# Optimization experiments

Measured on AMD Instinct MI355X. Metric: run time of the kernel, lower is better.

The kernel has to match this reference:

```python
import jax, jax.numpy as jnp
import numpy as np

IN_FEATURES = 1024
OUT_FEATURES = 1024
GRID_SIZE = 5
SPLINE_ORDER = 3
GRID_RANGE = (-1.0, 1.0)


def make_grid():
    h = (GRID_RANGE[1] - GRID_RANGE[0]) / GRID_SIZE
    knots = jnp.arange(-SPLINE_ORDER, GRID_SIZE + SPLINE_ORDER + 1, dtype=jnp.float32) * h + GRID_RANGE[0]
    return jnp.broadcast_to(knots, (IN_FEATURES, knots.shape[0]))  # (in, 12)


def b_splines(x, knots, p):
    # x: (B, in); knots: (in, nk). Cox-de Boor recursion, degree p.
    xs = x[:, :, None]                                   # (B, in, 1)
    bases = ((xs >= knots[None, :, :-1]) & (xs < knots[None, :, 1:])).astype(x.dtype)
    for k in range(1, p + 1):
        den1 = knots[:, k:-1] - knots[:, :-(k + 1)]
        den1 = jnp.where(den1 == 0, jnp.float32(1e-8), den1)
        den2 = knots[:, k + 1:] - knots[:, 1:-k]
        den2 = jnp.where(den2 == 0, jnp.float32(1e-8), den2)
        term1 = (xs - knots[None, :, :-(k + 1)]) / den1[None] * bases[:, :, :-1]
        term2 = (knots[None, :, k + 1:] - xs) / den2[None] * bases[:, :, 1:]
        bases = term1 + term2
    return bases  # (B, in, grid_size + p)


def setup_inputs() -> dict:
    key = jax.random.key(0)
    k1, k2, k3, k4 = jax.random.split(key, 4)
    K = GRID_SIZE + SPLINE_ORDER
    x = jax.random.normal(k1, (4096, IN_FEATURES), dtype=jnp.float32)
    base_weight = jax.random.normal(k2, (OUT_FEATURES, IN_FEATURES), dtype=jnp.float32) * (1.0 / np.sqrt(IN_FEATURES))
    spline_weight = jax.random.normal(k3, (OUT_FEATURES, IN_FEATURES, K), dtype=jnp.float32) * 0.02
    spline_scaler = jax.random.normal(k4, (OUT_FEATURES, IN_FEATURES), dtype=jnp.float32) * (1.0 / np.sqrt(IN_FEATURES))
    grid = make_grid()
    return {"x": x, "base_weight": base_weight, "spline_weight": spline_weight,
            "spline_scaler": spline_scaler, "grid": grid}


def reference(x, base_weight, spline_weight, spline_scaler, grid):
    base_out = jax.nn.silu(x) @ base_weight.T                      # (B, out)
    bases = b_splines(x, grid, SPLINE_ORDER)                       # (B, in, K)
    scaled_sw = spline_weight * spline_scaler[:, :, None]          # (out, in, K)
    spline_out = jnp.einsum('bik,oik->bo', bases, scaled_sw)       # (B, out)
    return base_out + spline_out
```

## Files before the change

### kernel.cpp

```cpp
#include <hip/hip_runtime.h>
#include <hip/hip_bf16.h>
#include <cstdint>
#include <cstddef>

#define AS1 __attribute__((address_space(1)))
#define AS3 __attribute__((address_space(3)))

typedef __bf16 bf16;
typedef __bf16 bf16x4 __attribute__((ext_vector_type(4)));
typedef __bf16 bf16x8 __attribute__((ext_vector_type(8)));
typedef float f32x4 __attribute__((ext_vector_type(4)));

static constexpr int M_ROWS = 4096;
static constexpr int N_COLS = 1024;
static constexpr int IN_F   = 1024;
static constexpr int K2     = IN_F * 9;
static constexpr int BK     = 32;
static constexpr int KT_CNT = K2 / BK;

static constexpr int GBK = 64;
static constexpr int GKT = K2 / GBK;


__device__ __forceinline__ void bases8(float x, float w8[8]) {
  float mf = x * 2.5f + 5.5f;
  int   m  = (int)floorf(mf);
  float u  = mf - (float)m;
  float u2 = u * u, u3 = u2 * u;
  float omu = 1.0f - u;
  const float s = 1.0f / 6.0f;
  float p0 = u3 * s;
  float p1 = (-3.f*u3 + 3.f*u2 + 3.f*u + 1.f) * s;
  float p2 = (3.f*u3 - 6.f*u2 + 4.f) * s;
  float p3 = omu * omu * omu * s;
  bool in = (m >= 0) && (m < 11);
#pragma unroll
  for (int j = 0; j < 8; ++j) {
    float v = 0.0f;
    v = (j == m)     ? p0 : v;
    v = (j == m - 1) ? p1 : v;
    v = (j == m - 2) ? p2 : v;
    v = (j == m - 3) ? p3 : v;
    w8[j] = in ? v : 0.0f;
  }
}

__global__ __launch_bounds__(256) void prep4(
    const float* __restrict__ x, const float* __restrict__ bw,
    const float* __restrict__ sw, const float* __restrict__ sc,
    bf16* __restrict__ A, bf16* __restrict__ BT) {
  const int bid = blockIdx.x;
  if (bid < (M_ROWS * IN_F) / (4 * 256)) {
    const int t  = bid * 256 + threadIdx.x;
    const int b  = t >> 8;
    const int i0 = (t & 255) * 4;
    const float4 xv4 = *(const float4*)(x + (size_t)b * IN_F + i0);
    const float xs[4] = {xv4.x, xv4.y, xv4.z, xv4.w};

    bf16x4 sil;
    bf16* arow = A + (size_t)b * K2;
#pragma unroll
    for (int j = 0; j < 4; ++j) {
      float xv = xs[j];
      sil[j] = (bf16)(xv / (1.0f + __expf(-xv)));
      float w8[8];
      bases8(xv, w8);
      bf16x8 outv;
#pragma unroll
      for (int k = 0; k < 8; ++k) outv[k] = (bf16)w8[k];
      *(bf16x8*)(arow + IN_F + (size_t)(i0 + j) * 8) = outv;
    }
    *(bf16x4*)(arow + i0) = sil;
  } else {
    const int t  = (bid - (M_ROWS * IN_F) / (4 * 256)) * 256 + threadIdx.x;
    const int o  = t >> 8;
    const int i0 = (t & 255) * 4;
    const float4 bv4 = *(const float4*)(bw + (size_t)o * IN_F + i0);
    const float4 sc4 = *(const float4*)(sc + (size_t)o * IN_F + i0);
    const float bs[4] = {bv4.x, bv4.y, bv4.z, bv4.w};
    const float ss[4] = {sc4.x, sc4.y, sc4.z, sc4.w};

    bf16x4 base;
    bf16* brow = BT + (size_t)o * K2;
#pragma unroll
    for (int j = 0; j < 4; ++j) {
      base[j] = (bf16)bs[j];
      const float4* swp = (const float4*)(sw + ((size_t)o * IN_F + i0 + j) * 8);
      float4 a = swp[0], c = swp[1];
      float wv[8] = {a.x, a.y, a.z, a.w, c.x, c.y, c.z, c.w};
      bf16x8 r;
#pragma unroll
      for (int k = 0; k < 8; ++k) r[k] = (bf16)(wv[k] * ss[j]);
      *(bf16x8*)(brow + IN_F + (size_t)(i0 + j) * 8) = r;
    }
    *(bf16x4*)(brow + i0) = base;
  }
}

__device__ __forceinline__ void expand_body(const float* __restrict__ x,
                                            bf16* __restrict__ A, int gid, int r0) {
  int b = gid >> 10;
  int i = gid & 1023;
  float xv = x[(size_t)r0 * IN_F + (size_t)gid];
  A[(size_t)b * K2 + i] = (bf16)(xv / (1.0f + __expf(-xv)));
  float w8[8];
  bases8(xv, w8);
  bf16x8 outv;
#pragma unroll
  for (int j = 0; j < 8; ++j) outv[j] = (bf16)w8[j];
  *(bf16x8*)(A + (size_t)b * K2 + IN_F + (size_t)i * 8) = outv;
}

__device__ __forceinline__ void makebt_body(const float* __restrict__ bw,
                                            const float* __restrict__ sw,
                                            const float* __restrict__ sc,
                                            bf16* __restrict__ BT, int gid) {
  int o = gid >> 10;
  int i = gid & 1023;
  BT[(size_t)o * K2 + i] = (bf16)bw[gid];
  float scale = sc[gid];
  const float4* swp = (const float4*)(sw + (size_t)gid * 8);
  float4 a = swp[0], b4 = swp[1];
  float wv[8] = {a.x, a.y, a.z, a.w, b4.x, b4.y, b4.z, b4.w};
  bf16x8 r;
#pragma unroll
  for (int j = 0; j < 8; ++j) r[j] = (bf16)(wv[j] * scale);
  *(bf16x8*)(BT + (size_t)o * K2 + IN_F + (size_t)i * 8) = r;
}

__global__ void expand_a(const float* __restrict__ x, bf16* __restrict__ A, int r0) {
  expand_body(x, A, blockIdx.x * blockDim.x + threadIdx.x, r0);
}
__global__ void make_bt(const float* __restrict__ bw, const float* __restrict__ sw,
                        const float* __restrict__ sc, bf16* __restrict__ BT) {
  makebt_body(bw, sw, sc, BT, blockIdx.x * blockDim.x + threadIdx.x);
}

__global__ __launch_bounds__(512, 2) void gemm256_8p(
    const bf16* __restrict__ A, const bf16* __restrict__ BT,
    float* __restrict__ P, int kt_seg) {
  __shared__ bf16 As[2][256 * GBK];
  __shared__ bf16 Bs[2][256 * GBK];

  const int tid  = threadIdx.x;
  const int lane = tid & 63;
  const int w    = tid >> 6;

  const int b     = blockIdx.x;
  const int mtile = b & 15;
  const int np    = (b >> 4) & 3;
  const int seg   = b >> 6;
  const int row0  = mtile * 256;
  const int col0  = np * 256;
  const int kt0   = seg * kt_seg;
  float* __restrict__ dst = P + (size_t)seg * M_ROWS * N_COLS;

  const int srow = lane >> 3;
  const int sch  = ((lane & 7) ^ srow) * 8;

  const int r  = lane & 15;
  const int q  = lane >> 4;
  const int wm = (w >> 2) * 128;
  const int wn = (w & 3) * 64;
  const int kc0 = ((0 + q) ^ (r & 7)) * 8;
  const int kc1 = ((4 + q) ^ (r & 7)) * 8;

  const bf16* aB = A  + (size_t)row0 * K2;
  const bf16* bB = BT + (size_t)col0 * K2;

  f32x4 acc[8][4];
#pragma unroll
  for (int mt = 0; mt < 8; ++mt)
#pragma unroll
    for (int nt = 0; nt < 4; ++nt)
      acc[mt][nt] = f32x4{0.f, 0.f, 0.f, 0.f};

  auto stageA = [&](int sbuf, int h, int kt) {
#pragma unroll
    for (int t8 = 0; t8 < 2; ++t8) {
      const int rg = h * 128 + w * 16 + t8 * 8;
      const bf16* ga = aB + (size_t)(rg + srow) * K2 + kt * GBK + sch;
      __builtin_amdgcn_global_load_lds((const AS1 void*)ga,
                                       (AS3 void*)&As[sbuf][rg * GBK], 16, 0, 0);
    }
  };
  auto stageB = [&](int sbuf, int h, int kt) {
#pragma unroll
    for (int t8 = 0; t8 < 2; ++t8) {
      const int rg = h * 128 + w * 16 + t8 * 8;
      const bf16* gb = bB + (size_t)(rg + srow) * K2 + kt * GBK + sch;
      __builtin_amdgcn_global_load_lds((const AS1 void*)gb,
                                       (AS3 void*)&Bs[sbuf][rg * GBK], 16, 0, 0);
    }
  };

  stageA(0, 0, kt0); stageA(0, 1, kt0);
  stageB(0, 0, kt0); stageB(0, 1, kt0);
  if (kt_seg > 1) stageA(1, 0, kt0 + 1);
  if (kt_seg > 1) asm volatile("s_waitcnt vmcnt(2)" ::: "memory");
  else            asm volatile("s_waitcnt vmcnt(0)" ::: "memory");
  __builtin_amdgcn_s_barrier();

  bf16x8 af[4][2], bfr[4][2];

  for (int t = 0; t < kt_seg; ++t) {
    const int buf = t & 1, nbuf = buf ^ 1;
    const bf16* as = As[buf];
    const bf16* bs = Bs[buf];
    const bool sN = (t + 1 < kt_seg);

#pragma unroll
    for (int j = 0; j < 4; ++j) {
      const bf16* ar = &as[(wm + j * 16 + r) * GBK];
      af[j][0] = *(const bf16x8*)&ar[kc0];
      af[j][1] = *(const bf16x8*)&ar[kc1];
    }
#pragma unroll
    for (int j = 0; j < 2; ++j) {
      const bf16* br = &bs[(wn + j * 16 + r) * GBK];
      bfr[j][0] = *(const bf16x8*)&br[kc0];
      bfr[j][1] = *(const bf16x8*)&br[kc1];
    }
    if (sN) stageA(nbuf, 1, kt0 + t + 1);
    asm volatile("s_waitcnt lgkmcnt(8)" ::: "memory");
    __builtin_amdgcn_s_barrier();
    asm volatile("s_waitcnt lgkmcnt(0)" ::: "memory");
    __builtin_amdgcn_sched_barrier(0);
    __builtin_amdgcn_s_setprio(1);
#pragma unroll
    for (int j = 0; j < 4; ++j)
#pragma unroll
      for (int n = 0; n < 2; ++n) {
        acc[j][n] = __builtin_amdgcn_mfma_f32_16x16x32_bf16(af[j][0], bfr[n][0], acc[j][n], 0, 0, 0);
        acc[j][n] = __builtin_amdgcn_mfma_f32_16x16x32_bf16(af[j][1], bfr[n][1], acc[j][n], 0, 0, 0);
      }
    __builtin_amdgcn_s_setprio(0);
    __builtin_amdgcn_s_barrier();

#pragma unroll
    for (int j = 0; j < 2; ++j) {
      const bf16* br = &bs[(wn + (2 + j) * 16 + r) * GBK];
      bfr[2 + j][0] = *(const bf16x8*)&br[kc0];
      bfr[2 + j][1] = *(const bf16x8*)&br[kc1];
    }
    if (sN) stageB(nbuf, 0, kt0 + t + 1);
    __builtin_amdgcn_s_barrier();
    asm volatile("s_waitcnt lgkmcnt(0)" ::: "memory");
    __builtin_amdgcn_sched_barrier(0);
    __builtin_amdgcn_s_setprio(1);
#pragma unroll
    for (int j = 0; j < 4; ++j)
#pragma unroll
      for (int n = 0; n < 2; ++n) {
        acc[j][2 + n] = __builtin_amdgcn_mfma_f32_16x16x32_bf16(af[j][0], bfr[2 + n][0], acc[j][2 + n], 0, 0, 0);
        acc[j][2 + n] = __builtin_amdgcn_mfma_f32_16x16x32_bf16(af[j][1], bfr[2 + n][1], acc[j][2 + n], 0, 0, 0);
      }
    __builtin_amdgcn_s_setprio(0);
    __builtin_amdgcn_s_barrier();

#pragma unroll
    for (int j = 0; j < 4; ++j) {
      const bf16* ar = &as[(wm + (4 + j) * 16 + r) * GBK];
      af[j][0] = *(const bf16x8*)&ar[kc0];
      af[j][1] = *(const bf16x8*)&ar[kc1];
    }
    if (sN) stageB(nbuf, 1, kt0 + t + 1);
    __builtin_amdgcn_s_barrier();
    asm volatile("s_waitcnt lgkmcnt(0)" ::: "memory");
    __builtin_amdgcn_sched_barrier(0);
    __builtin_amdgcn_s_setprio(1);
#pragma unroll
    for (int j = 0; j < 4; ++j)
#pragma unroll
      for (int n = 0; n < 2; ++n) {
        acc[4 + j][n] = __builtin_amdgcn_mfma_f32_16x16x32_bf16(af[j][0], bfr[n][0], acc[4 + j][n], 0, 0, 0);
        acc[4 + j][n] = __builtin_amdgcn_mfma_f32_16x16x32_bf16(af[j][1], bfr[n][1], acc[4 + j][n], 0, 0, 0);
      }
    __builtin_amdgcn_s_setprio(0);
    __builtin_amdgcn_s_barrier();

    if (t + 2 < kt_seg) stageA(buf, 0, kt0 + t + 2);
    if (sN) {
      if (t + 2 < kt_seg) asm volatile("s_waitcnt vmcnt(2)" ::: "memory");
      else                asm volatile("s_waitcnt vmcnt(0)" ::: "memory");
    }
    __builtin_amdgcn_s_barrier();
    __builtin_amdgcn_s_setprio(1);
#pragma unroll
    for (int j = 0; j < 4; ++j)
#pragma unroll
      for (int n = 0; n < 2; ++n) {
        acc[4 + j][2 + n] = __builtin_amdgcn_mfma_f32_16x16x32_bf16(af[j][0], bfr[2 + n][0], acc[4 + j][2 + n], 0, 0, 0);
        acc[4 + j][2 + n] = __builtin_amdgcn_mfma_f32_16x16x32_bf16(af[j][1], bfr[2 + n][1], acc[4 + j][2 + n], 0, 0, 0);
      }
    __builtin_amdgcn_s_setprio(0);
    __builtin_amdgcn_s_barrier();
  }

#pragma unroll
  for (int mt = 0; mt < 8; ++mt)
#pragma unroll
    for (int nt = 0; nt < 4; ++nt)
#pragma unroll
      for (int k = 0; k < 4; ++k) {
        int row = row0 + wm + mt * 16 + q * 4 + k;
        int col = col0 + wn + nt * 16 + r;
        dst[(size_t)row * N_COLS + col] = acc[mt][nt][k];
      }
}

__global__ __launch_bounds__(256, 2) void gemm_fused(
    const bf16* __restrict__ A, const bf16* __restrict__ BT,
    float* __restrict__ d0, float* __restrict__ d1,
    int r0, int mt_cnt, int kt_seg) {
  __shared__ bf16 As[2][128 * GBK];
  __shared__ bf16 Bs[2][128 * GBK];

  const int tid  = threadIdx.x;
  const int lane = tid & 63;
  const int w    = tid >> 6;

  const int bps = mt_cnt * 8;
  int b   = blockIdx.x;
  const int seg = b / bps;
  b -= seg * bps;
  const int row0 = (b % mt_cnt) * 128;
  const int col0 = (b / mt_cnt) * 128;
  float* __restrict__ dst = seg ? d1 : d0;
  const int kt0 = seg * kt_seg;

  const int srow = lane >> 3;
  const int sch  = ((lane & 7) ^ srow) * 8;
  const int r  = lane & 15;
  const int q  = lane >> 4;
  const int wm = (w >> 1) * 64;
  const int wn = (w & 1) * 64;
  const int kc0 = ((0 + q) ^ (r & 7)) * 8;
  const int kc1 = ((4 + q) ^ (r & 7)) * 8;

  const bf16* aB = A  + (size_t)row0 * K2;
  const bf16* bB = BT + (size_t)col0 * K2;

  f32x4 acc[4][4];
#pragma unroll
  for (int mt = 0; mt < 4; ++mt)
#pragma unroll
    for (int nt = 0; nt < 4; ++nt)
      acc[mt][nt] = f32x4{0.f, 0.f, 0.f, 0.f};

  auto stage = [&](int sbuf, int kt) {
#pragma unroll
    for (int t = 0; t < 4; ++t) {
      const int rg = w * 32 + t * 8;
      const bf16* ga = aB + (size_t)(rg + srow) * K2 + kt * GBK + sch;
      __builtin_amdgcn_global_load_lds((const AS1 void*)ga,
                                       (AS3 void*)&As[sbuf][rg * GBK], 16, 0, 0);
      const bf16* gb = bB + (size_t)(rg + srow) * K2 + kt * GBK + sch;
      __builtin_amdgcn_global_load_lds((const AS1 void*)gb,
                                       (AS3 void*)&Bs[sbuf][rg * GBK], 16, 0, 0);
    }
  };

  stage(0, kt0);
  int buf = 0;
  for (int i = 0; i < kt_seg; ++i) {
    if (i + 1 < kt_seg) {
      stage(buf ^ 1, kt0 + i + 1);
      asm volatile("s_waitcnt vmcnt(8)" ::: "memory");
    } else {
      asm volatile("s_waitcnt vmcnt(0)" ::: "memory");
    }
    __builtin_amdgcn_s_barrier();
    __builtin_amdgcn_sched_barrier(0);

    const bf16* as = As[buf];
    const bf16* bs = Bs[buf];

#pragma unroll
    for (int kk = 0; kk < 2; ++kk) {
      const int kc = kk ? kc1 : kc0;
      bf16x8 af[4], bfr[4];
#pragma unroll
      for (int mt = 0; mt < 4; ++mt)
        af[mt] = *(const bf16x8*)&as[(wm + mt * 16 + r) * GBK + kc];
#pragma unroll
      for (int nt = 0; nt < 4; ++nt)
        bfr[nt] = *(const bf16x8*)&bs[(wn + nt * 16 + r) * GBK + kc];
#pragma unroll
      for (int mt = 0; mt < 4; ++mt)
#pragma unroll
        for (int nt = 0; nt < 4; ++nt)
          acc[mt][nt] = __builtin_amdgcn_mfma_f32_16x16x32_bf16(
              af[mt], bfr[nt], acc[mt][nt], 0, 0, 0);
    }
    __builtin_amdgcn_s_barrier();
    buf ^= 1;
  }

#pragma unroll
  for (int mt = 0; mt < 4; ++mt)
#pragma unroll
    for (int nt = 0; nt < 4; ++nt)
#pragma unroll
      for (int k = 0; k < 4; ++k) {
        int row = r0 + row0 + wm + mt * 16 + q * 4 + k;
        int col = col0 + wn + nt * 16 + r;
        dst[(size_t)row * N_COLS + col] = acc[mt][nt][k];
      }
}

__global__ __launch_bounds__(256) void reduce_addN(
    const float* __restrict__ P, float* __restrict__ out, int segs) {
  const size_t plane = (size_t)M_ROWS * N_COLS / 4;
  const f32x4* p = (const f32x4*)P;
  f32x4* o = (f32x4*)out;
  const size_t stride = (size_t)gridDim.x * blockDim.x;
  for (size_t i = (size_t)blockIdx.x * blockDim.x + threadIdx.x; i < plane;
       i += stride) {
    if (segs == 4) {
      f32x4 a = p[i] + p[plane + i];
      f32x4 c = p[2 * plane + i] + p[3 * plane + i];
      o[i] = a + c;
    } else {
      f32x4 a = p[i];
      for (int s = 1; s < segs; ++s) a += p[(size_t)s * plane + i];
      o[i] = a;
    }
  }
}

__global__ __launch_bounds__(256) void kan_fused_fallback(
    const float* __restrict__ x, const float* __restrict__ bw,
    const float* __restrict__ sw, const float* __restrict__ sc,
    float* __restrict__ out) {
  __shared__ bf16 As[64 * BK];
  __shared__ bf16 Bs[128 * BK];
  const int tid  = threadIdx.x;
  const int lane = tid & 63;
  const int w    = tid >> 6;
  const int col0 = blockIdx.x * 128;
  const int row0 = blockIdx.y * 64;
  const int srow = tid >> 2, sq = tid & 3;
  const int r = lane & 15, q = lane >> 4, wn = w * 32;

  f32x4 acc[4][2];
#pragma unroll
  for (int mt = 0; mt < 4; ++mt)
#pragma unroll
    for (int nt = 0; nt < 2; ++nt) acc[mt][nt] = f32x4{0,0,0,0};

  for (int kt = 0; kt < KT_CNT; ++kt) {
    if (kt < 32) {
      const int cc = sq * 8;
      const float4* xp = (const float4*)(x + (size_t)(row0+srow)*IN_F + kt*BK + cc);
      float4 a = xp[0], b4 = xp[1];
      float xv[8] = {a.x,a.y,a.z,a.w,b4.x,b4.y,b4.z,b4.w};
      bf16x8 av;
#pragma unroll
      for (int j = 0; j < 8; ++j) av[j] = (bf16)(xv[j] / (1.0f + __expf(-xv[j])));
      *(bf16x8*)&As[srow * BK + cc] = av;
#pragma unroll
      for (int h = 0; h < 2; ++h) {
        const float4* bp = (const float4*)(bw + (size_t)(col0+h*64+srow)*IN_F + kt*BK + cc);
        float4 c0 = bp[0], c1 = bp[1];
        float bv[8] = {c0.x,c0.y,c0.z,c0.w,c1.x,c1.y,c1.z,c1.w};
        bf16x8 bb;
#pragma unroll
        for (int j = 0; j < 8; ++j) bb[j] = (bf16)bv[j];
        *(bf16x8*)&Bs[(h*64+srow)*BK + cc] = bb;
      }
    } else {
      const int i = (kt - 32) * 4 + sq;
      float xv = x[(size_t)(row0+srow)*IN_F + i];
      float w8[8]; bases8(xv, w8);
      bf16x8 av;
#pragma unroll
      for (int j = 0; j < 8; ++j) av[j] = (bf16)w8[j];
      *(bf16x8*)&As[srow * BK + sq * 8] = av;
#pragma unroll
      for (int h = 0; h < 2; ++h) {
        const int o = col0 + h*64 + srow;
        float s1 = sc[(size_t)o*IN_F + i];
        const float4* sp = (const float4*)(sw + ((size_t)o*IN_F + i)*8);
        float4 c0 = sp[0], c1 = sp[1];
        float wv[8] = {c0.x,c0.y,c0.z,c0.w,c1.x,c1.y,c1.z,c1.w};
        bf16x8 bb;
#pragma unroll
        for (int j = 0; j < 8; ++j) bb[j] = (bf16)(wv[j]*s1);
        *(bf16x8*)&Bs[(h*64+srow)*BK + sq*8] = bb;
      }
    }
    __syncthreads();
    bf16x8 af[4], bfr[2];
#pragma unroll
    for (int mt = 0; mt < 4; ++mt)
      af[mt] = *(const bf16x8*)&As[(mt*16+r)*BK + q*8];
#pragma unroll
    for (int nt = 0; nt < 2; ++nt)
      bfr[nt] = *(const bf16x8*)&Bs[(wn+nt*16+r)*BK + q*8];
#pragma unroll
    for (int mt = 0; mt < 4; ++mt)
#pragma unroll
      for (int nt = 0; nt < 2; ++nt)
        acc[mt][nt] = __builtin_amdgcn_mfma_f32_16x16x32_bf16(af[mt], bfr[nt], acc[mt][nt], 0,0,0);
    __syncthreads();
  }
#pragma unroll
  for (int mt = 0; mt < 4; ++mt)
#pragma unroll
    for (int nt = 0; nt < 2; ++nt)
#pragma unroll
      for (int k = 0; k < 4; ++k)
        out[(size_t)(row0+mt*16+q*4+k)*N_COLS + col0+wn+nt*16+r] = acc[mt][nt][k];
}

extern "C" void kernel_launch(void* const* d_in, const int* in_sizes, int n_in,
                              void* d_out, int out_size, void* d_ws, size_t ws_size,
                              hipStream_t stream) {
  const float* x    = (const float*)d_in[0];
  const float* bw   = (const float*)d_in[1];
  const float* sw   = (const float*)d_in[2];
  const float* sc   = (const float*)d_in[3];
  float* out = (float*)d_out;

  const size_t BT_BYTES  = (size_t)N_COLS * K2 * sizeof(bf16);
  const size_t ROW_BYTES = (size_t)K2 * sizeof(bf16);
  const size_t A_BYTES   = (size_t)M_ROWS * ROW_BYTES;
  const size_t OUT_BYTES = (size_t)M_ROWS * N_COLS * sizeof(float);

  int S = 0;
  for (int c = 4; c >= 2; --c)
    if (GKT % c == 0 && BT_BYTES + A_BYTES + (size_t)c * OUT_BYTES <= ws_size) {
      S = c; break;
    }

  if (S >= 2) {
    bf16*  BT    = (bf16*)d_ws;
    bf16*  Aslab = BT + (size_t)N_COLS * K2;
    float* P     = (float*)((char*)d_ws + BT_BYTES + A_BYTES);
    prep4<<<(M_ROWS * IN_F) / (4 * 256) + (N_COLS * IN_F) / (4 * 256), 256, 0,
            stream>>>(x, bw, sw, sc, Aslab, BT);
    gemm256_8p<<<S * 64, 512, 0, stream>>>(Aslab, BT, P, GKT / S);
    reduce_addN<<<2048, 256, 0, stream>>>(P, out, S);
  } else {
    int SL = 0;
    for (int cand = 4096; cand >= 128; cand >>= 1)
      if (BT_BYTES + (size_t)cand * ROW_BYTES <= ws_size) { SL = cand; break; }
    if (SL) {
      bf16* BT    = (bf16*)d_ws;
      bf16* Aslab = BT + (size_t)N_COLS * K2;
      make_bt<<<(N_COLS * IN_F) / 256, 256, 0, stream>>>(bw, sw, sc, BT);
      for (int r0 = 0; r0 < M_ROWS; r0 += SL) {
        expand_a<<<(SL * IN_F) / 256, 256, 0, stream>>>(x, Aslab, r0);
        gemm_fused<<<(SL / 128) * (N_COLS / 128), 256, 0, stream>>>(
            Aslab, BT, out, out, r0, SL / 128, GKT);
      }
    } else {
      kan_fused_fallback<<<dim3(N_COLS / 128, M_ROWS / 64), 256, 0, stream>>>(
          x, bw, sw, sc, out);
    }
  }
  (void)in_sizes; (void)n_in; (void)out_size;
}
```

Baseline: 211.6 us.

## Merge prep, GEMM and reduction into one cooperative kernel with grid syncs

Replaces the three-launch sequence (prep, split-K GEMM, reduce) with a single cooperative kernel that uses grid-wide syncs between phases. The prep phase becomes a grid-stride loop over the fixed cooperative grid of S*64 blocks of 512 threads. The aim is to remove launch gaps and inter-kernel drain. The cost is a prep and reduce phase that run on far fewer threads than their dedicated launches had, plus grid-sync overhead. The old three-kernel path remains as a fallback if the cooperative launch is unsupported or fails.

```diff
diff --git a/kernel.cpp b/kernel.cpp
--- a/kernel.cpp
+++ b/kernel.cpp
@@ -1,10 +1,13 @@
 #include <hip/hip_runtime.h>
+#include <hip/hip_cooperative_groups.h>
 #include <hip/hip_bf16.h>
 #include <cstdint>
 #include <cstddef>
 
 #define AS1 __attribute__((address_space(1)))
 #define AS3 __attribute__((address_space(3)))
+
+namespace cg = cooperative_groups;
 
 typedef __bf16 bf16;
 typedef __bf16 bf16x4 __attribute__((ext_vector_type(4)));
@@ -45,98 +48,69 @@
   }
 }
 
-__global__ __launch_bounds__(256) void prep4(
+__device__ __forceinline__ void expand4(const float* __restrict__ x,
+                                        bf16* __restrict__ A, int t) {
+  const int b  = t >> 8;
+  const int i0 = (t & 255) * 4;
+  const float4 xv4 = *(const float4*)(x + (size_t)b * IN_F + i0);
+  const float xs[4] = {xv4.x, xv4.y, xv4.z, xv4.w};
+
+  bf16x4 sil;
+  bf16* arow = A + (size_t)b * K2;
+#pragma unroll
+  for (int j = 0; j < 4; ++j) {
+    float xv = xs[j];
+    sil[j] = (bf16)(xv / (1.0f + __expf(-xv)));
+    float w8[8];
+    bases8(xv, w8);
+    bf16x8 outv;
+#pragma unroll
+    for (int k = 0; k < 8; ++k) outv[k] = (bf16)w8[k];
+    *(bf16x8*)(arow + IN_F + (size_t)(i0 + j) * 8) = outv;
+  }
+  *(bf16x4*)(arow + i0) = sil;
+}
+
+__device__ __forceinline__ void makebt4(const float* __restrict__ bw,
+                                        const float* __restrict__ sw,
+                                        const float* __restrict__ sc,
+                                        bf16* __restrict__ BT, int t) {
+  const int o  = t >> 8;
+  const int i0 = (t & 255) * 4;
+  const float4 bv4 = *(const float4*)(bw + (size_t)o * IN_F + i0);
+  const float4 sc4 = *(const float4*)(sc + (size_t)o * IN_F + i0);
+  const float bs[4] = {bv4.x, bv4.y, bv4.z, bv4.w};
+  const float ss[4] = {sc4.x, sc4.y, sc4.z, sc4.w};
+
+  bf16x4 base;
+  bf16* brow = BT + (size_t)o * K2;
+#pragma unroll
+  for (int j = 0; j < 4; ++j) {
+    base[j] = (bf16)bs[j];
+    const float4* swp = (const float4*)(sw + ((size_t)o * IN_F + i0 + j) * 8);
+    float4 a = swp[0], c = swp[1];
+    float wv[8] = {a.x, a.y, a.z, a.w, c.x, c.y, c.z, c.w};
+    bf16x8 r;
+#pragma unroll
+    for (int k = 0; k < 8; ++k) r[k] = (bf16)(wv[k] * ss[j]);
+    *(bf16x8*)(brow + IN_F + (size_t)(i0 + j) * 8) = r;
+  }
+  *(bf16x4*)(brow + i0) = base;
+}
+
+__device__ __forceinline__ void prep_body(
     const float* __restrict__ x, const float* __restrict__ bw,
     const float* __restrict__ sw, const float* __restrict__ sc,
     bf16* __restrict__ A, bf16* __restrict__ BT) {
-  const int bid = blockIdx.x;
-  if (bid < (M_ROWS * IN_F) / (4 * 256)) {
-    const int t  = bid * 256 + threadIdx.x;
-    const int b  = t >> 8;
-    const int i0 = (t & 255) * 4;
-    const float4 xv4 = *(const float4*)(x + (size_t)b * IN_F + i0);
-    const float xs[4] = {xv4.x, xv4.y, xv4.z, xv4.w};
-
-    bf16x4 sil;
-    bf16* arow = A + (size_t)b * K2;
-#pragma unroll
-    for (int j = 0; j < 4; ++j) {
-      float xv = xs[j];
-      sil[j] = (bf16)(xv / (1.0f + __expf(-xv)));
-      float w8[8];
-      bases8(xv, w8);
-      bf16x8 outv;
-#pragma unroll
-      for (int k = 0; k < 8; ++k) outv[k] = (bf16)w8[k];
-      *(bf16x8*)(arow + IN_F + (size_t)(i0 + j) * 8) = outv;
-    }
-    *(bf16x4*)(arow + i0) = sil;
-  } else {
-    const int t  = (bid - (M_ROWS * IN_F) / (4 * 256)) * 256 + threadIdx.x;
-    const int o  = t >> 8;
-    const int i0 = (t & 255) * 4;
-    const float4 bv4 = *(const float4*)(bw + (size_t)o * IN_F + i0);
-    const float4 sc4 = *(const float4*)(sc + (size_t)o * IN_F + i0);
-    const float bs[4] = {bv4.x, bv4.y, bv4.z, bv4.w};
-    const float ss[4] = {sc4.x, sc4.y, sc4.z, sc4.w};
-
-    bf16x4 base;
-    bf16* brow = BT + (size_t)o * K2;
-#pragma unroll
-    for (int j = 0; j < 4; ++j) {
-      base[j] = (bf16)bs[j];
-      const float4* swp = (const float4*)(sw + ((size_t)o * IN_F + i0 + j) * 8);
-      float4 a = swp[0], c = swp[1];
-      float wv[8] = {a.x, a.y, a.z, a.w, c.x, c.y, c.z, c.w};
-      bf16x8 r;
-#pragma unroll
-      for (int k = 0; k < 8; ++k) r[k] = (bf16)(wv[k] * ss[j]);
-      *(bf16x8*)(brow + IN_F + (size_t)(i0 + j) * 8) = r;
-    }
-    *(bf16x4*)(brow + i0) = base;
-  }
-}
-
-__device__ __forceinline__ void expand_body(const float* __restrict__ x,
-                                            bf16* __restrict__ A, int gid, int r0) {
-  int b = gid >> 10;
-  int i = gid & 1023;
-  float xv = x[(size_t)r0 * IN_F + (size_t)gid];
-  A[(size_t)b * K2 + i] = (bf16)(xv / (1.0f + __expf(-xv)));
-  float w8[8];
-  bases8(xv, w8);
-  bf16x8 outv;
-#pragma unroll
-  for (int j = 0; j < 8; ++j) outv[j] = (bf16)w8[j];
-  *(bf16x8*)(A + (size_t)b * K2 + IN_F + (size_t)i * 8) = outv;
-}
-
-__device__ __forceinline__ void makebt_body(const float* __restrict__ bw,
-                                            const float* __restrict__ sw,
-                                            const float* __restrict__ sc,
-                                            bf16* __restrict__ BT, int gid) {
-  int o = gid >> 10;
-  int i = gid & 1023;
-  BT[(size_t)o * K2 + i] = (bf16)bw[gid];
-  float scale = sc[gid];
-  const float4* swp = (const float4*)(sw + (size_t)gid * 8);
-  float4 a = swp[0], b4 = swp[1];
-  float wv[8] = {a.x, a.y, a.z, a.w, b4.x, b4.y, b4.z, b4.w};
-  bf16x8 r;
-#pragma unroll
-  for (int j = 0; j < 8; ++j) r[j] = (bf16)(wv[j] * scale);
-  *(bf16x8*)(BT + (size_t)o * K2 + IN_F + (size_t)i * 8) = r;
-}
-
-__global__ void expand_a(const float* __restrict__ x, bf16* __restrict__ A, int r0) {
-  expand_body(x, A, blockIdx.x * blockDim.x + threadIdx.x, r0);
-}
-__global__ void make_bt(const float* __restrict__ bw, const float* __restrict__ sw,
-                        const float* __restrict__ sc, bf16* __restrict__ BT) {
-  makebt_body(bw, sw, sc, BT, blockIdx.x * blockDim.x + threadIdx.x);
-}
-
-__global__ __launch_bounds__(512, 2) void gemm256_8p(
+  const int nthr = gridDim.x * blockDim.x;
+  const int tid0 = blockIdx.x * blockDim.x + threadIdx.x;
+  const int NE = (M_ROWS * IN_F) / 4;
+  const int NB = (N_COLS * IN_F) / 4;
+  for (int t = tid0; t < NE; t += nthr) expand4(x, A, t);
+  for (int t = tid0; t < NB; t += nthr) makebt4(bw, sw, sc, BT, t);
+}
+
+__device__ __forceinline__ void gemm256_body(
     const bf16* __restrict__ A, const bf16* __restrict__ BT,
     float* __restrict__ P, int kt_seg) {
   __shared__ bf16 As[2][256 * GBK];
@@ -309,108 +283,8 @@
       }
 }
 
-__global__ __launch_bounds__(256, 2) void gemm_fused(
-    const bf16* __restrict__ A, const bf16* __restrict__ BT,
-    float* __restrict__ d0, float* __restrict__ d1,
-    int r0, int mt_cnt, int kt_seg) {
-  __shared__ bf16 As[2][128 * GBK];
-  __shared__ bf16 Bs[2][128 * GBK];
-
-  const int tid  = threadIdx.x;
-  const int lane = tid & 63;
-  const int w    = tid >> 6;
-
-  const int bps = mt_cnt * 8;
-  int b   = blockIdx.x;
-  const int seg = b / bps;
-  b -= seg * bps;
-  const int row0 = (b % mt_cnt) * 128;
-  const int col0 = (b / mt_cnt) * 128;
-  float* __restrict__ dst = seg ? d1 : d0;
-  const int kt0 = seg * kt_seg;
-
-  const int srow = lane >> 3;
-  const int sch  = ((lane & 7) ^ srow) * 8;
-  const int r  = lane & 15;
-  const int q  = lane >> 4;
-  const int wm = (w >> 1) * 64;
-  const int wn = (w & 1) * 64;
-  const int kc0 = ((0 + q) ^ (r & 7)) * 8;
-  const int kc1 = ((4 + q) ^ (r & 7)) * 8;
-
-  const bf16* aB = A  + (size_t)row0 * K2;
-  const bf16* bB = BT + (size_t)col0 * K2;
-
-  f32x4 acc[4][4];
-#pragma unroll
-  for (int mt = 0; mt < 4; ++mt)
-#pragma unroll
-    for (int nt = 0; nt < 4; ++nt)
-      acc[mt][nt] = f32x4{0.f, 0.f, 0.f, 0.f};
-
-  auto stage = [&](int sbuf, int kt) {
-#pragma unroll
-    for (int t = 0; t < 4; ++t) {
-      const int rg = w * 32 + t * 8;
-      const bf16* ga = aB + (size_t)(rg + srow) * K2 + kt * GBK + sch;
-      __builtin_amdgcn_global_load_lds((const AS1 void*)ga,
-                                       (AS3 void*)&As[sbuf][rg * GBK], 16, 0, 0);
-      const bf16* gb = bB + (size_t)(rg + srow) * K2 + kt * GBK + sch;
-      __builtin_amdgcn_global_load_lds((const AS1 void*)gb,
-                                       (AS3 void*)&Bs[sbuf][rg * GBK], 16, 0, 0);
-    }
-  };
-
-  stage(0, kt0);
-  int buf = 0;
-  for (int i = 0; i < kt_seg; ++i) {
-    if (i + 1 < kt_seg) {
-      stage(buf ^ 1, kt0 + i + 1);
-      asm volatile("s_waitcnt vmcnt(8)" ::: "memory");
-    } else {
-      asm volatile("s_waitcnt vmcnt(0)" ::: "memory");
-    }
-    __builtin_amdgcn_s_barrier();
-    __builtin_amdgcn_sched_barrier(0);
-
-    const bf16* as = As[buf];
-    const bf16* bs = Bs[buf];
-
-#pragma unroll
-    for (int kk = 0; kk < 2; ++kk) {
-      const int kc = kk ? kc1 : kc0;
-      bf16x8 af[4], bfr[4];
-#pragma unroll
-      for (int mt = 0; mt < 4; ++mt)
-        af[mt] = *(const bf16x8*)&as[(wm + mt * 16 + r) * GBK + kc];
-#pragma unroll
-      for (int nt = 0; nt < 4; ++nt)
-        bfr[nt] = *(const bf16x8*)&bs[(wn + nt * 16 + r) * GBK + kc];
-#pragma unroll
-      for (int mt = 0; mt < 4; ++mt)
-#pragma unroll
-        for (int nt = 0; nt < 4; ++nt)
-          acc[mt][nt] = __builtin_amdgcn_mfma_f32_16x16x32_bf16(
-              af[mt], bfr[nt], acc[mt][nt], 0, 0, 0);
-    }
-    __builtin_amdgcn_s_barrier();
-    buf ^= 1;
-  }
-
-#pragma unroll
-  for (int mt = 0; mt < 4; ++mt)
-#pragma unroll
-    for (int nt = 0; nt < 4; ++nt)
-#pragma unroll
-      for (int k = 0; k < 4; ++k) {
-        int row = r0 + row0 + wm + mt * 16 + q * 4 + k;
-        int col = col0 + wn + nt * 16 + r;
-        dst[(size_t)row * N_COLS + col] = acc[mt][nt][k];
-      }
-}
-
-__global__ __launch_bounds__(256) void reduce_addN(
-    const float* __restrict__ P, float* __restrict__ out, int segs) {
+__device__ __forceinline__ void reduce_body(const float* __restrict__ P,
+                                            float* __restrict__ out, int segs) {
   const size_t plane = (size_t)M_ROWS * N_COLS / 4;
   const f32x4* p = (const f32x4*)P;
   f32x4* o = (f32x4*)out;
@@ -429,6 +303,175 @@
   }
 }
 
+__global__ __launch_bounds__(512, 2) void kan_mono(
+    const float* __restrict__ x, const float* __restrict__ bw,
+    const float* __restrict__ sw, const float* __restrict__ sc,
+    bf16* __restrict__ A, bf16* __restrict__ BT,
+    float* __restrict__ P, float* __restrict__ out, int kt_seg) {
+  prep_body(x, bw, sw, sc, A, BT);
+  cg::this_grid().sync();
+  gemm256_body(A, BT, P, kt_seg);
+  cg::this_grid().sync();
+  reduce_body(P, out, gridDim.x >> 6);
+}
+
+__global__ __launch_bounds__(512) void prep4(
+    const float* __restrict__ x, const float* __restrict__ bw,
+    const float* __restrict__ sw, const float* __restrict__ sc,
+    bf16* __restrict__ A, bf16* __restrict__ BT) {
+  prep_body(x, bw, sw, sc, A, BT);
+}
+
+__global__ __launch_bounds__(512, 2) void gemm256_8p(
+    const bf16* __restrict__ A, const bf16* __restrict__ BT,
+    float* __restrict__ P, int kt_seg) {
+  gemm256_body(A, BT, P, kt_seg);
+}
+
+__global__ __launch_bounds__(256) void reduce_addN(
+    const float* __restrict__ P, float* __restrict__ out, int segs) {
+  reduce_body(P, out, segs);
+}
+
+__device__ __forceinline__ void expand_body(const float* __restrict__ x,
+                                            bf16* __restrict__ A, int gid, int r0) {
+  int b = gid >> 10;
+  int i = gid & 1023;
+  float xv = x[(size_t)r0 * IN_F + (size_t)gid];
+  A[(size_t)b * K2 + i] = (bf16)(xv / (1.0f + __expf(-xv)));
+  float w8[8];
+  bases8(xv, w8);
+  bf16x8 outv;
+#pragma unroll
+  for (int j = 0; j < 8; ++j) outv[j] = (bf16)w8[j];
+  *(bf16x8*)(A + (size_t)b * K2 + IN_F + (size_t)i * 8) = outv;
+}
+
+__device__ __forceinline__ void makebt_body(const float* __restrict__ bw,
+                                            const float* __restrict__ sw,
+                                            const float* __restrict__ sc,
+                                            bf16* __restrict__ BT, int gid) {
+  int o = gid >> 10;
+  int i = gid & 1023;
+  BT[(size_t)o * K2 + i] = (bf16)bw[gid];
+  float scale = sc[gid];
+  const float4* swp = (const float4*)(sw + (size_t)gid * 8);
+  float4 a = swp[0], b4 = swp[1];
+  float wv[8] = {a.x, a.y, a.z, a.w, b4.x, b4.y, b4.z, b4.w};
+  bf16x8 r;
+#pragma unroll
+  for (int j = 0; j < 8; ++j) r[j] = (bf16)(wv[j] * scale);
+  *(bf16x8*)(BT + (size_t)o * K2 + IN_F + (size_t)i * 8) = r;
+}
+
+__global__ void expand_a(const float* __restrict__ x, bf16* __restrict__ A, int r0) {
+  expand_body(x, A, blockIdx.x * blockDim.x + threadIdx.x, r0);
+}
+__global__ void make_bt(const float* __restrict__ bw, const float* __restrict__ sw,
+                        const float* __restrict__ sc, bf16* __restrict__ BT) {
+  makebt_body(bw, sw, sc, BT, blockIdx.x * blockDim.x + threadIdx.x);
+}
+
+__global__ __launch_bounds__(256, 2) void gemm_fused(
+    const bf16* __restrict__ A, const bf16* __restrict__ BT,
+    float* __restrict__ d0, float* __restrict__ d1,
+    int r0, int mt_cnt, int kt_seg) {
+  __shared__ bf16 As[2][128 * GBK];
+  __shared__ bf16 Bs[2][128 * GBK];
+
+  const int tid  = threadIdx.x;
+  const int lane = tid & 63;
+  const int w    = tid >> 6;
+
+  const int bps = mt_cnt * 8;
+  int b   = blockIdx.x;
+  const int seg = b / bps;
+  b -= seg * bps;
+  const int row0 = (b % mt_cnt) * 128;
+  const int col0 = (b / mt_cnt) * 128;
+  float* __restrict__ dst = seg ? d1 : d0;
+  const int kt0 = seg * kt_seg;
+
+  const int srow = lane >> 3;
+  const int sch  = ((lane & 7) ^ srow) * 8;
+  const int r  = lane & 15;
+  const int q  = lane >> 4;
+  const int wm = (w >> 1) * 64;
+  const int wn = (w & 1) * 64;
+  const int kc0 = ((0 + q) ^ (r & 7)) * 8;
+  const int kc1 = ((4 + q) ^ (r & 7)) * 8;
+
+  const bf16* aB = A  + (size_t)row0 * K2;
+  const bf16* bB = BT + (size_t)col0 * K2;
+
+  f32x4 acc[4][4];
+#pragma unroll
+  for (int mt = 0; mt < 4; ++mt)
+#pragma unroll
+    for (int nt = 0; nt < 4; ++nt)
+      acc[mt][nt] = f32x4{0.f, 0.f, 0.f, 0.f};
+
+  auto stage = [&](int sbuf, int kt) {
+#pragma unroll
+    for (int t = 0; t < 4; ++t) {
+      const int rg = w * 32 + t * 8;
+      const bf16* ga = aB + (size_t)(rg + srow) * K2 + kt * GBK + sch;
+      __builtin_amdgcn_global_load_lds((const AS1 void*)ga,
+                                       (AS3 void*)&As[sbuf][rg * GBK], 16, 0, 0);
+      const bf16* gb = bB + (size_t)(rg + srow) * K2 + kt * GBK + sch;
+      __builtin_amdgcn_global_load_lds((const AS1 void*)gb,
+                                       (AS3 void*)&Bs[sbuf][rg * GBK], 16, 0, 0);
+    }
+  };
+
+  stage(0, kt0);
+  int buf = 0;
+  for (int i = 0; i < kt_seg; ++i) {
+    if (i + 1 < kt_seg) {
+      stage(buf ^ 1, kt0 + i + 1);
+      asm volatile("s_waitcnt vmcnt(8)" ::: "memory");
+    } else {
+      asm volatile("s_waitcnt vmcnt(0)" ::: "memory");
+    }
+    __builtin_amdgcn_s_barrier();
+    __builtin_amdgcn_sched_barrier(0);
+
+    const bf16* as = As[buf];
+    const bf16* bs = Bs[buf];
+
+#pragma unroll
+    for (int kk = 0; kk < 2; ++kk) {
+      const int kc = kk ? kc1 : kc0;
+      bf16x8 af[4], bfr[4];
+#pragma unroll
+      for (int mt = 0; mt < 4; ++mt)
+        af[mt] = *(const bf16x8*)&as[(wm + mt * 16 + r) * GBK + kc];
+#pragma unroll
+      for (int nt = 0; nt < 4; ++nt)
+        bfr[nt] = *(const bf16x8*)&bs[(wn + nt * 16 + r) * GBK + kc];
+#pragma unroll
+      for (int mt = 0; mt < 4; ++mt)
+#pragma unroll
+        for (int nt = 0; nt < 4; ++nt)
+          acc[mt][nt] = __builtin_amdgcn_mfma_f32_16x16x32_bf16(
+              af[mt], bfr[nt], acc[mt][nt], 0, 0, 0);
+    }
+    __builtin_amdgcn_s_barrier();
+    buf ^= 1;
+  }
+
+#pragma unroll
+  for (int mt = 0; mt < 4; ++mt)
+#pragma unroll
+    for (int nt = 0; nt < 4; ++nt)
+#pragma unroll
+      for (int k = 0; k < 4; ++k) {
+        int row = r0 + row0 + wm + mt * 16 + q * 4 + k;
+        int col = col0 + wn + nt * 16 + r;
+        dst[(size_t)row * N_COLS + col] = acc[mt][nt][k];
+      }
+}
+
 __global__ __launch_bounds__(256) void kan_fused_fallback(
     const float* __restrict__ x, const float* __restrict__ bw,
     const float* __restrict__ sw, const float* __restrict__ sc,
@@ -538,10 +581,31 @@
     bf16*  BT    = (bf16*)d_ws;
     bf16*  Aslab = BT + (size_t)N_COLS * K2;
     float* P     = (float*)((char*)d_ws + BT_BYTES + A_BYTES);
-    prep4<<<(M_ROWS * IN_F) / (4 * 256) + (N_COLS * IN_F) / (4 * 256), 256, 0,
-            stream>>>(x, bw, sw, sc, Aslab, BT);
-    gemm256_8p<<<S * 64, 512, 0, stream>>>(Aslab, BT, P, GKT / S);
-    reduce_addN<<<2048, 256, 0, stream>>>(P, out, S);
+    int kt_seg = GKT / S;
+
+    static int coop = -1;
+    if (coop < 0) {
+      int v = 0, dev = 0;
+      (void)hipGetDevice(&dev);
+      if (hipDeviceGetAttribute(&v, hipDeviceAttributeCooperativeLaunch, dev) !=
+          hipSuccess)
+        v = 0;
+      coop = v;
+    }
+
+    hipError_t ce = hipErrorUnknown;
+    if (coop == 1) {
+      void* args[] = {(void*)&x, (void*)&bw, (void*)&sw, (void*)&sc,
+                      (void*)&Aslab, (void*)&BT, (void*)&P, (void*)&out,
+                      (void*)&kt_seg};
+      ce = hipLaunchCooperativeKernel((const void*)kan_mono, dim3(S * 64),
+                                      dim3(512), args, 0, stream);
+    }
+    if (ce != hipSuccess) {
+      prep4<<<256, 512, 0, stream>>>(x, bw, sw, sc, Aslab, BT);
+      gemm256_8p<<<S * 64, 512, 0, stream>>>(Aslab, BT, P, kt_seg);
+      reduce_addN<<<2048, 256, 0, stream>>>(P, out, S);
+    }
   } else {
     int SL = 0;
     for (int cand = 4096; cand >= 128; cand >>= 1)
```

Result: slower. 306.9 us (+45.1%).
